# Kernel tuning notes

Hardware: AMD Instinct MI355X
Metric: run time of the kernel (lower is better)

The kernel has to match this reference:

```python
import jax, jax.numpy as jnp
import numpy as np

IGNORE_INDEX = -100
BT, H, V = 2048, 4096, 32000


def setup_inputs() -> dict:
    key = jax.random.key(0)
    k1, k2, k3, k4 = jax.random.split(key, 4)
    _input = jax.random.normal(k1, (BT, H), dtype=jnp.float32) * 0.02
    lin_weight = jax.random.normal(k2, (V, H), dtype=jnp.float32) * 0.02
    bias = jnp.zeros((V,), dtype=jnp.float32)
    target = jax.random.randint(k3, (BT,), 0, V)
    loss_weights = jax.random.uniform(k4, (BT,), dtype=jnp.float32)
    reduce_sum_loss_weights = jnp.sum(loss_weights)  # scalar float32
    return {
        "lin_weight": lin_weight,
        "_input": _input,
        "target": target,
        "bias": bias,
        "loss_weights": loss_weights,
        "reduce_sum_loss_weights": reduce_sum_loss_weights,
        "grad_accumulation_steps": 1,
    }


def reference(lin_weight, _input, target, bias, loss_weights,
              reduce_sum_loss_weights, grad_accumulation_steps):
    # logits: (BT, V) -- the torch module chunks over BT to avoid materializing
    # this; as a correctness reference we compute it directly.
    logits = _input @ lin_weight.T + bias
    mask = target != IGNORE_INDEX                      # (BT,)
    n_non_ignore = jnp.maximum(mask.sum(), 1).astype(logits.dtype)
    safe_t = jnp.where(mask, target, 0)
    lse = jax.nn.logsumexp(logits, axis=-1)            # (BT,)
    gold = jnp.take_along_axis(logits, safe_t[:, None], axis=-1)[:, 0]
    # liger kernel with reduction='mean' divides per-row loss by n_non_ignore
    loss_1d = jnp.where(mask, (lse - gold) / n_non_ignore, 0.0)
    total = jnp.sum(loss_1d * loss_weights)
    rs = jnp.asarray(reduce_sum_loss_weights).reshape(())
    denom = jnp.where(rs == 0, 1.0, rs)
    loss = jnp.where(rs == 0, 0.0, total / denom)
    return loss / grad_accumulation_steps
```

## Files before the change

### kernel.cpp

```cpp
#include <hip/hip_runtime.h>
#include <hip/hip_bf16.h>
#include <math.h>

#define IGNORE_INDEX (-100)

constexpr int BT = 2048, H = 4096, V = 32000;
constexpr int BM = 256, BN = 256, BK = 64;
constexpr int KT = H / BK;
constexpr int MT2 = BT / BM;
constexpr int NT2 = V / BN;
constexpr int NCHUNK = NT2 * 4;

typedef int   i32x4  __attribute__((ext_vector_type(4)));
typedef int   i32x8  __attribute__((ext_vector_type(8)));
typedef float f32x16 __attribute__((ext_vector_type(16)));

#define SC8 120

__device__ __forceinline__ void gload_lds16(const char* g, char* l) {
  __builtin_amdgcn_global_load_lds(
      (const __attribute__((address_space(1))) unsigned int*)(g),
      (__attribute__((address_space(3))) unsigned int*)(l), 16, 0, 0);
}

#define BAR()        asm volatile("s_barrier" ::: "memory")
#define WAIT_VM(N)   asm volatile("s_waitcnt vmcnt(" #N ")" ::: "memory")

__global__ __launch_bounds__(256)
void convert_fp8(const float* __restrict__ src, char* __restrict__ dst,
                 int n8) {
  int i = blockIdx.x * blockDim.x + threadIdx.x;
  const int stride = gridDim.x * blockDim.x;
  for (; i < n8; i += stride) {
    const float4 f0 = ((const float4*)src)[2 * i];
    const float4 f1 = ((const float4*)src)[2 * i + 1];
    const float S = 128.f;
    int lo = 0, hi = 0;
    lo = __builtin_amdgcn_cvt_pk_fp8_f32(f0.x * S, f0.y * S, lo, false);
    lo = __builtin_amdgcn_cvt_pk_fp8_f32(f0.z * S, f0.w * S, lo, true);
    hi = __builtin_amdgcn_cvt_pk_fp8_f32(f1.x * S, f1.y * S, hi, false);
    hi = __builtin_amdgcn_cvt_pk_fp8_f32(f1.z * S, f1.w * S, hi, true);
    int2 v; v.x = lo; v.y = hi;
    ((int2*)dst)[i] = v;
  }
}

__global__ __launch_bounds__(512, 2)
void gemm_lse_fp8(const char* __restrict__ Wq,
                  const char* __restrict__ Xq,
                  const int* __restrict__ target,
                  const float* __restrict__ bias,
                  float* __restrict__ pM, float* __restrict__ pS,
                  float* __restrict__ gold)
{
  __shared__ char As[32768];
  __shared__ char Bs[32768];

  const int tid  = threadIdx.x;
  const int lane = tid & 63;
  const int wid  = tid >> 6;
  const int wr   = wid >> 2;
  const int wcol = wid & 3;

  const int bid = (int)blockIdx.x;
  const int swz = (bid & 7) * 125 + (bid >> 3);
  const int mt = swz & (MT2 - 1);
  const int nt = swz >> 3;
  const int m0 = mt * BM, n0 = nt * BN;

  const int l31 = lane & 31;
  const int h   = lane >> 5;
  const int r2  = (l31 >> 1) & 3;
  const int s0  = ((2 * h) ^ r2) << 4;
  const int s1  = ((2 * h + 1) ^ r2) << 4;
  const int abase = (wr * 128 + l31) * 64;
  const int bbase = (wcol * 64 + l31) * 64;

  const int srow  = lane >> 2;
  const int sslot = ((lane & 3) ^ ((lane >> 3) & 3)) << 4;

  const char* asrc = Xq + (size_t)(m0 + wid * 32 + srow) * H + sslot;
  const char* bsrc = Wq + (size_t)(n0 + wid * 32 + srow) * H + sslot;

  f32x16 acc[4][2] = {};
  i32x8 aF0, aF1, bF0, bF1;

#define STAGE_A(BUF, DT)                                                      \
  { gload_lds16(asrc + (DT) * BK,                                             \
                &As[(BUF) * 16384 + wid * 2048 + lane * 16]);                 \
    gload_lds16(asrc + (size_t)16 * H + (DT) * BK,                            \
                &As[(BUF) * 16384 + wid * 2048 + 1024 + lane * 16]); }

#define STAGE_B(BUF, DT)                                                      \
  { gload_lds16(bsrc + (DT) * BK,                                             \
                &Bs[(BUF) * 16384 + wid * 2048 + lane * 16]);                 \
    gload_lds16(bsrc + (size_t)16 * H + (DT) * BK,                            \
                &Bs[(BUF) * 16384 + wid * 2048 + 1024 + lane * 16]); }

#define RDA(DST, BUF, MI)                                                     \
  { i32x4 lo = *(const i32x4*)&As[(BUF) * 16384 + abase + (MI) * 2048 + s0];  \
    i32x4 hi = *(const i32x4*)&As[(BUF) * 16384 + abase + (MI) * 2048 + s1];  \
    DST[0] = lo[0]; DST[1] = lo[1]; DST[2] = lo[2]; DST[3] = lo[3];           \
    DST[4] = hi[0]; DST[5] = hi[1]; DST[6] = hi[2]; DST[7] = hi[3]; }

#define RDB(DST, BUF, NJ)                                                     \
  { i32x4 lo = *(const i32x4*)&Bs[(BUF) * 16384 + bbase + (NJ) * 2048 + s0];  \
    i32x4 hi = *(const i32x4*)&Bs[(BUF) * 16384 + bbase + (NJ) * 2048 + s1];  \
    DST[0] = lo[0]; DST[1] = lo[1]; DST[2] = lo[2]; DST[3] = lo[3];           \
    DST[4] = hi[0]; DST[5] = hi[1]; DST[6] = hi[2]; DST[7] = hi[3]; }

#define MFMA4(MH)                                                             \
  { __builtin_amdgcn_s_setprio(1);                                            \
    acc[(MH)*2+0][0] = __builtin_amdgcn_mfma_scale_f32_32x32x64_f8f6f4(       \
        aF0, bF0, acc[(MH)*2+0][0], 0, 0, 0, SC8, 0, SC8);                    \
    acc[(MH)*2+0][1] = __builtin_amdgcn_mfma_scale_f32_32x32x64_f8f6f4(       \
        aF0, bF1, acc[(MH)*2+0][1], 0, 0, 0, SC8, 0, SC8);                    \
    acc[(MH)*2+1][0] = __builtin_amdgcn_mfma_scale_f32_32x32x64_f8f6f4(       \
        aF1, bF0, acc[(MH)*2+1][0], 0, 0, 0, SC8, 0, SC8);                    \
    acc[(MH)*2+1][1] = __builtin_amdgcn_mfma_scale_f32_32x32x64_f8f6f4(       \
        aF1, bF1, acc[(MH)*2+1][1], 0, 0, 0, SC8, 0, SC8);                    \
    __builtin_amdgcn_s_setprio(0); }

  STAGE_B(0, 0); STAGE_A(0, 0);

  for (int t = 0; t <= KT - 4; t += 2) {
    STAGE_B(1, 1);
    WAIT_VM(2); BAR();
    RDA(aF0, 0, 0); RDA(aF1, 0, 1); RDB(bF0, 0, 0); RDB(bF1, 0, 1);
    MFMA4(0);
    STAGE_A(1, 1);
    WAIT_VM(2); BAR();
    RDA(aF0, 0, 2); RDA(aF1, 0, 3);
    MFMA4(1);
    STAGE_B(0, 2);
    WAIT_VM(2); BAR();
    RDA(aF0, 1, 0); RDA(aF1, 1, 1); RDB(bF0, 1, 0); RDB(bF1, 1, 1);
    MFMA4(0);
    STAGE_A(0, 2);
    WAIT_VM(2); BAR();
    RDA(aF0, 1, 2); RDA(aF1, 1, 3);
    MFMA4(1);

    asrc += 2 * BK; bsrc += 2 * BK;
  }

  STAGE_B(1, 1);
  WAIT_VM(2); BAR();
  RDA(aF0, 0, 0); RDA(aF1, 0, 1); RDB(bF0, 0, 0); RDB(bF1, 0, 1);
  MFMA4(0);
  STAGE_A(1, 1);
  WAIT_VM(2); BAR();
  RDA(aF0, 0, 2); RDA(aF1, 0, 3);
  MFMA4(1);
  WAIT_VM(0); BAR();
  RDA(aF0, 1, 0); RDA(aF1, 1, 1); RDB(bF0, 1, 0); RDB(bF1, 1, 1);
  MFMA4(0);
  RDA(aF0, 1, 2); RDA(aF1, 1, 3);
  MFMA4(1);

#undef STAGE_A
#undef STAGE_B
#undef RDA
#undef RDB
#undef MFMA4

  const int colbase = n0 + wcol * 64;
  float bv[2];
#pragma unroll
  for (int nj = 0; nj < 2; ++nj) bv[nj] = bias[colbase + nj * 32 + l31];

  const int chunk = nt * 4 + wcol;
#pragma unroll
  for (int mi = 0; mi < 4; ++mi) {
#pragma unroll
    for (int r = 0; r < 16; ++r) {
      const int row = m0 + wr * 128 + mi * 32 + (r & 3) + 8 * (r >> 2) + 4 * h;
      const float v0 = acc[mi][0][r] + bv[0];
      const float v1 = acc[mi][1][r] + bv[1];
      float mx = fmaxf(v0, v1);
#pragma unroll
      for (int d = 1; d < 32; d <<= 1) mx = fmaxf(mx, __shfl_xor(mx, d));
      float s = expf(v0 - mx) + expf(v1 - mx);
#pragma unroll
      for (int d = 1; d < 32; d <<= 1) s += __shfl_xor(s, d);
      if (l31 == 0) {
        pM[(size_t)row * NCHUNK + chunk] = mx;
        pS[(size_t)row * NCHUNK + chunk] = s;
      }
      const int t = target[row];
      const int d0 = t - colbase;
      if (d0 >= 0 && d0 < 64 && l31 == (d0 & 31)) {
        gold[row] = (d0 >> 5) ? v1 : v0;
      }
    }
  }
}

__global__ __launch_bounds__(256)
void reduce_lse(const float* __restrict__ pM, const float* __restrict__ pS,
                const float* __restrict__ gold, const int* __restrict__ target,
                const float* __restrict__ lw, float* __restrict__ rowterm)
{
  const int wid = threadIdx.x >> 6, lane = threadIdx.x & 63;
  const int row = blockIdx.x * 4 + wid;
  if (row >= BT) return;
  const float* pm = pM + (size_t)row * NCHUNK;
  const float* ps = pS + (size_t)row * NCHUNK;
  float m = -INFINITY;
  for (int c2 = lane; c2 < NCHUNK; c2 += 64) m = fmaxf(m, pm[c2]);
#pragma unroll
  for (int d = 1; d < 64; d <<= 1) m = fmaxf(m, __shfl_xor(m, d));
  float s = 0.f;
  for (int c2 = lane; c2 < NCHUNK; c2 += 64) s += ps[c2] * expf(pm[c2] - m);
#pragma unroll
  for (int d = 1; d < 64; d <<= 1) s += __shfl_xor(s, d);
  if (lane == 0) {
    const int t = target[row];
    float term = 0.f;
    if (t != IGNORE_INDEX) term = (m + logf(s) - gold[row]) * lw[row];
    rowterm[row] = term;
  }
}

__global__ __launch_bounds__(256)
void finalize(const float* __restrict__ rowterm, const int* __restrict__ target,
              const float* __restrict__ rsw, const int* __restrict__ gas,
              float* __restrict__ out)
{
  __shared__ float sred[4];
  __shared__ int cred[4];
  const int tid = threadIdx.x;
  float s = 0.f;
  int cnt = 0;
  for (int i = tid; i < BT; i += 256) {
    s += rowterm[i];
    cnt += (target[i] != IGNORE_INDEX) ? 1 : 0;
  }
#pragma unroll
  for (int d = 1; d < 64; d <<= 1) {
    s += __shfl_xor(s, d);
    cnt += __shfl_xor(cnt, d);
  }
  const int wid = tid >> 6, lane = tid & 63;
  if (lane == 0) { sred[wid] = s; cred[wid] = cnt; }
  __syncthreads();
  if (tid == 0) {
    const float st = sred[0] + sred[1] + sred[2] + sred[3];
    const int ct = cred[0] + cred[1] + cred[2] + cred[3];
    const float n = (float)((ct > 0) ? ct : 1);
    const float rs = rsw[0];
    float loss = (rs == 0.f) ? 0.f : (st / n) / rs;
    loss /= (float)gas[0];
    out[0] = loss;
  }
}

extern "C" void kernel_launch(void* const* d_in, const int* in_sizes, int n_in,
                              void* d_out, int out_size, void* d_ws, size_t ws_size,
                              hipStream_t stream)
{
  const float* Wt     = (const float*)d_in[0];
  const float* X      = (const float*)d_in[1];
  const int*   target = (const int*)d_in[2];
  const float* bias   = (const float*)d_in[3];
  const float* lw     = (const float*)d_in[4];
  const float* rsw    = (const float*)d_in[5];
  const int*   gas    = (const int*)d_in[6];
  float* out = (float*)d_out;

  const size_t nW = (size_t)V * H, nX = (size_t)BT * H;

  char* Wq = (char*)d_ws;
  char* Xq = Wq + nW;
  float* pM = (float*)(Xq + nX);
  float* pS = pM + (size_t)BT * NCHUNK;
  float* gold = pS + (size_t)BT * NCHUNK;
  float* rowterm = gold + BT;

  convert_fp8<<<dim3(2048), dim3(256), 0, stream>>>(Wt, Wq, (int)(nW / 8));
  convert_fp8<<<dim3(256), dim3(256), 0, stream>>>(X, Xq, (int)(nX / 8));
  gemm_lse_fp8<<<dim3(MT2 * NT2), dim3(512), 0, stream>>>(Wq, Xq, target,
                                                          bias, pM, pS, gold);
  reduce_lse<<<dim3(BT / 4), dim3(256), 0, stream>>>(pM, pS, gold, target, lw,
                                                     rowterm);
  finalize<<<dim3(1), dim3(256), 0, stream>>>(rowterm, target, rsw, gas, out);
}
```

Before: 549.0 us.

## Load A operand directly from pre-tiled fp8 global layout, bypassing LDS

The X conversion kernel now writes fp8 data in an MFMA-fragment-tiled layout, so each lane can read its A fragment straight from global memory as contiguous 32-byte loads. The GEMM drops the A shared-memory buffer and its staging, keeps only B in LDS, and double-buffers A fragments in registers, prefetching them one K step ahead. This aims to cut LDS traffic and barriers, at the cost of more registers (two sets of four i32x8 A fragments) and global-load latency exposure on A. Since the A tile is reused by many blocks, it relies on L2 hits.

```diff
diff --git a/kernel.cpp b/kernel.cpp
--- a/kernel.cpp
+++ b/kernel.cpp
@@ -25,6 +25,7 @@
 
 #define BAR()        asm volatile("s_barrier" ::: "memory")
 #define WAIT_VM(N)   asm volatile("s_waitcnt vmcnt(" #N ")" ::: "memory")
+#define SB0()        __builtin_amdgcn_sched_barrier(0)
 
 __global__ __launch_bounds__(256)
 void convert_fp8(const float* __restrict__ src, char* __restrict__ dst,
@@ -45,15 +46,38 @@
   }
 }
 
+__global__ __launch_bounds__(256)
+void convert_x_fp8_tiled(const float* __restrict__ src,
+                         char* __restrict__ dst, int n8) {
+  int i = blockIdx.x * blockDim.x + threadIdx.x;
+  const int stride = gridDim.x * blockDim.x;
+  for (; i < n8; i += stride) {
+    const float4 f0 = ((const float4*)src)[2 * i];
+    const float4 f1 = ((const float4*)src)[2 * i + 1];
+    const float S = 128.f;
+    int lo = 0, hi = 0;
+    lo = __builtin_amdgcn_cvt_pk_fp8_f32(f0.x * S, f0.y * S, lo, false);
+    lo = __builtin_amdgcn_cvt_pk_fp8_f32(f0.z * S, f0.w * S, lo, true);
+    hi = __builtin_amdgcn_cvt_pk_fp8_f32(f1.x * S, f1.y * S, hi, false);
+    hi = __builtin_amdgcn_cvt_pk_fp8_f32(f1.z * S, f1.w * S, hi, true);
+    int2 v; v.x = lo; v.y = hi;
+    const int r  = i >> 9;
+    const int k0 = (i & 511) * 8;
+    const int lane = (r & 31) + ((k0 >> 5) & 1) * 32;
+    const size_t addr =
+        ((size_t)((r >> 5) * 64 + (k0 >> 6)) * 64 + lane) * 32 + (k0 & 31);
+    *(int2*)(dst + addr) = v;
+  }
+}
+
 __global__ __launch_bounds__(512, 2)
-void gemm_lse_fp8(const char* __restrict__ Wq,
-                  const char* __restrict__ Xq,
-                  const int* __restrict__ target,
-                  const float* __restrict__ bias,
-                  float* __restrict__ pM, float* __restrict__ pS,
-                  float* __restrict__ gold)
-{
-  __shared__ char As[32768];
+void gemm_lse_adirect(const char* __restrict__ Wq,
+                      const char* __restrict__ Xt,
+                      const int* __restrict__ target,
+                      const float* __restrict__ bias,
+                      float* __restrict__ pM, float* __restrict__ pS,
+                      float* __restrict__ gold)
+{
   __shared__ char Bs[32768];
 
   const int tid  = threadIdx.x;
@@ -73,35 +97,23 @@
   const int r2  = (l31 >> 1) & 3;
   const int s0  = ((2 * h) ^ r2) << 4;
   const int s1  = ((2 * h + 1) ^ r2) << 4;
-  const int abase = (wr * 128 + l31) * 64;
   const int bbase = (wcol * 64 + l31) * 64;
 
   const int srow  = lane >> 2;
   const int sslot = ((lane & 3) ^ ((lane >> 3) & 3)) << 4;
-
-  const char* asrc = Xq + (size_t)(m0 + wid * 32 + srow) * H + sslot;
   const char* bsrc = Wq + (size_t)(n0 + wid * 32 + srow) * H + sslot;
 
-  f32x16 acc[4][2] = {};
-  i32x8 aF0, aF1, bF0, bF1;
-
-#define STAGE_A(BUF, DT)                                                      \
-  { gload_lds16(asrc + (DT) * BK,                                             \
-                &As[(BUF) * 16384 + wid * 2048 + lane * 16]);                 \
-    gload_lds16(asrc + (size_t)16 * H + (DT) * BK,                            \
-                &As[(BUF) * 16384 + wid * 2048 + 1024 + lane * 16]); }
-
-#define STAGE_B(BUF, DT)                                                      \
-  { gload_lds16(bsrc + (DT) * BK,                                             \
+  const int rg0 = mt * 8 + wr * 4;
+  const int aoff = lane * 32;
+
+  f32x16 acc[8] = {};
+  i32x8 aC[4], aN[4], bF0, bF1;
+
+#define STAGE_B(BUF, T)                                                       \
+  { gload_lds16(bsrc + (T) * BK,                                              \
                 &Bs[(BUF) * 16384 + wid * 2048 + lane * 16]);                 \
-    gload_lds16(bsrc + (size_t)16 * H + (DT) * BK,                            \
+    gload_lds16(bsrc + (size_t)16 * H + (T) * BK,                             \
                 &Bs[(BUF) * 16384 + wid * 2048 + 1024 + lane * 16]); }
-
-#define RDA(DST, BUF, MI)                                                     \
-  { i32x4 lo = *(const i32x4*)&As[(BUF) * 16384 + abase + (MI) * 2048 + s0];  \
-    i32x4 hi = *(const i32x4*)&As[(BUF) * 16384 + abase + (MI) * 2048 + s1];  \
-    DST[0] = lo[0]; DST[1] = lo[1]; DST[2] = lo[2]; DST[3] = lo[3];           \
-    DST[4] = hi[0]; DST[5] = hi[1]; DST[6] = hi[2]; DST[7] = hi[3]; }
 
 #define RDB(DST, BUF, NJ)                                                     \
   { i32x4 lo = *(const i32x4*)&Bs[(BUF) * 16384 + bbase + (NJ) * 2048 + s0];  \
@@ -109,60 +121,56 @@
     DST[0] = lo[0]; DST[1] = lo[1]; DST[2] = lo[2]; DST[3] = lo[3];           \
     DST[4] = hi[0]; DST[5] = hi[1]; DST[6] = hi[2]; DST[7] = hi[3]; }
 
-#define MFMA4(MH)                                                             \
+#define LOADA(DST, T)                                                         \
+  { _Pragma("unroll")                                                         \
+    for (int mi = 0; mi < 4; ++mi) {                                          \
+      const char* ap = Xt + ((size_t)((rg0 + mi) * 64 + (T)) << 11) + aoff;   \
+      i32x4 lo = *(const i32x4*)(ap);                                         \
+      i32x4 hi = *(const i32x4*)(ap + 16);                                    \
+      DST[mi][0]=lo[0]; DST[mi][1]=lo[1]; DST[mi][2]=lo[2]; DST[mi][3]=lo[3]; \
+      DST[mi][4]=hi[0]; DST[mi][5]=hi[1]; DST[mi][6]=hi[2]; DST[mi][7]=hi[3]; \
+    } }
+
+#define MFMA8(ASET)                                                           \
   { __builtin_amdgcn_s_setprio(1);                                            \
-    acc[(MH)*2+0][0] = __builtin_amdgcn_mfma_scale_f32_32x32x64_f8f6f4(       \
-        aF0, bF0, acc[(MH)*2+0][0], 0, 0, 0, SC8, 0, SC8);                    \
-    acc[(MH)*2+0][1] = __builtin_amdgcn_mfma_scale_f32_32x32x64_f8f6f4(       \
-        aF0, bF1, acc[(MH)*2+0][1], 0, 0, 0, SC8, 0, SC8);                    \
-    acc[(MH)*2+1][0] = __builtin_amdgcn_mfma_scale_f32_32x32x64_f8f6f4(       \
-        aF1, bF0, acc[(MH)*2+1][0], 0, 0, 0, SC8, 0, SC8);                    \
-    acc[(MH)*2+1][1] = __builtin_amdgcn_mfma_scale_f32_32x32x64_f8f6f4(       \
-        aF1, bF1, acc[(MH)*2+1][1], 0, 0, 0, SC8, 0, SC8);                    \
+    _Pragma("unroll")                                                         \
+    for (int mi = 0; mi < 4; ++mi) {                                          \
+      acc[mi*2+0] = __builtin_amdgcn_mfma_scale_f32_32x32x64_f8f6f4(          \
+          ASET[mi], bF0, acc[mi*2+0], 0, 0, 0, SC8, 0, SC8);                  \
+      acc[mi*2+1] = __builtin_amdgcn_mfma_scale_f32_32x32x64_f8f6f4(          \
+          ASET[mi], bF1, acc[mi*2+1], 0, 0, 0, SC8, 0, SC8);                  \
+    }                                                                         \
     __builtin_amdgcn_s_setprio(0); }
 
-  STAGE_B(0, 0); STAGE_A(0, 0);
-
-  for (int t = 0; t <= KT - 4; t += 2) {
-    STAGE_B(1, 1);
-    WAIT_VM(2); BAR();
-    RDA(aF0, 0, 0); RDA(aF1, 0, 1); RDB(bF0, 0, 0); RDB(bF1, 0, 1);
-    MFMA4(0);
-    STAGE_A(1, 1);
-    WAIT_VM(2); BAR();
-    RDA(aF0, 0, 2); RDA(aF1, 0, 3);
-    MFMA4(1);
-    STAGE_B(0, 2);
-    WAIT_VM(2); BAR();
-    RDA(aF0, 1, 0); RDA(aF1, 1, 1); RDB(bF0, 1, 0); RDB(bF1, 1, 1);
-    MFMA4(0);
-    STAGE_A(0, 2);
-    WAIT_VM(2); BAR();
-    RDA(aF0, 1, 2); RDA(aF1, 1, 3);
-    MFMA4(1);
-
-    asrc += 2 * BK; bsrc += 2 * BK;
-  }
-
-  STAGE_B(1, 1);
-  WAIT_VM(2); BAR();
-  RDA(aF0, 0, 0); RDA(aF1, 0, 1); RDB(bF0, 0, 0); RDB(bF1, 0, 1);
-  MFMA4(0);
-  STAGE_A(1, 1);
-  WAIT_VM(2); BAR();
-  RDA(aF0, 0, 2); RDA(aF1, 0, 3);
-  MFMA4(1);
-  WAIT_VM(0); BAR();
-  RDA(aF0, 1, 0); RDA(aF1, 1, 1); RDB(bF0, 1, 0); RDB(bF1, 1, 1);
-  MFMA4(0);
-  RDA(aF0, 1, 2); RDA(aF1, 1, 3);
-  MFMA4(1);
-
-#undef STAGE_A
+  LOADA(aC, 0);
+  STAGE_B(0, 0);
+  WAIT_VM(0);
+  BAR();
+
+  for (int t = 0; t < KT - 2; t += 2) {
+    STAGE_B(1, t + 1);
+    RDB(bF0, 0, 0); RDB(bF1, 0, 1);
+    LOADA(aN, t + 1);
+    MFMA8(aC);
+    SB0(); WAIT_VM(8); BAR();
+    STAGE_B(0, t + 2);
+    RDB(bF0, 1, 0); RDB(bF1, 1, 1);
+    LOADA(aC, t + 2);
+    MFMA8(aN);
+    SB0(); WAIT_VM(8); BAR();
+  }
+  STAGE_B(1, KT - 1);
+  RDB(bF0, 0, 0); RDB(bF1, 0, 1);
+  LOADA(aN, KT - 1);
+  MFMA8(aC);
+  SB0(); WAIT_VM(8); BAR();
+  RDB(bF0, 1, 0); RDB(bF1, 1, 1);
+  MFMA8(aN);
+
 #undef STAGE_B
-#undef RDA
 #undef RDB
-#undef MFMA4
+#undef LOADA
+#undef MFMA8
 
   const int colbase = n0 + wcol * 64;
   float bv[2];
@@ -175,8 +183,8 @@
 #pragma unroll
     for (int r = 0; r < 16; ++r) {
       const int row = m0 + wr * 128 + mi * 32 + (r & 3) + 8 * (r >> 2) + 4 * h;
-      const float v0 = acc[mi][0][r] + bv[0];
-      const float v1 = acc[mi][1][r] + bv[1];
+      const float v0 = acc[mi * 2 + 0][r] + bv[0];
+      const float v1 = acc[mi * 2 + 1][r] + bv[1];
       float mx = fmaxf(v0, v1);
 #pragma unroll
       for (int d = 1; d < 32; d <<= 1) mx = fmaxf(mx, __shfl_xor(mx, d));
@@ -271,16 +279,18 @@
   const size_t nW = (size_t)V * H, nX = (size_t)BT * H;
 
   char* Wq = (char*)d_ws;
-  char* Xq = Wq + nW;
-  float* pM = (float*)(Xq + nX);
+  char* Xt = Wq + nW;
+  float* pM = (float*)(Xt + nX);
   float* pS = pM + (size_t)BT * NCHUNK;
   float* gold = pS + (size_t)BT * NCHUNK;
   float* rowterm = gold + BT;
 
   convert_fp8<<<dim3(2048), dim3(256), 0, stream>>>(Wt, Wq, (int)(nW / 8));
-  convert_fp8<<<dim3(256), dim3(256), 0, stream>>>(X, Xq, (int)(nX / 8));
-  gemm_lse_fp8<<<dim3(MT2 * NT2), dim3(512), 0, stream>>>(Wq, Xq, target,
-                                                          bias, pM, pS, gold);
+  convert_x_fp8_tiled<<<dim3(1024), dim3(256), 0, stream>>>(X, Xt,
+                                                            (int)(nX / 8));
+  gemm_lse_adirect<<<dim3(MT2 * NT2), dim3(512), 0, stream>>>(Wq, Xt, target,
+                                                              bias, pM, pS,
+                                                              gold);
   reduce_lse<<<dim3(BT / 4), dim3(256), 0, stream>>>(pM, pS, gold, target, lw,
                                                      rowterm);
   finalize<<<dim3(1), dim3(256), 0, stream>>>(rowterm, target, rsw, gas, out);
```

Result: slower. 565.6 us (+3.0%).

## Switch fp8 GEMM main loop to triple-buffered LDS pipeline with one barrier per stage

Applied to the files above, without the earlier changes.

The fused GEMM+logsumexp kernel moves from a two-slot LDS ring with a barrier per half-tile to a three-slot ring. Each K-step issues loads two tiles ahead, waits on vmcnt, runs all MFMAs for the current tile, then takes a single barrier. The goal is deeper prefetch and fewer barriers, so global-to-LDS latency is better hidden behind MFMA work. The cost is 96 KB of LDS per block instead of 64 KB, which may stop two 512-thread blocks from fitting per CU and so reduce occupancy.

```diff
diff --git a/kernel.cpp b/kernel.cpp
--- a/kernel.cpp
+++ b/kernel.cpp
@@ -25,6 +25,7 @@
 
 #define BAR()        asm volatile("s_barrier" ::: "memory")
 #define WAIT_VM(N)   asm volatile("s_waitcnt vmcnt(" #N ")" ::: "memory")
+#define SB0()        __builtin_amdgcn_sched_barrier(0)
 
 __global__ __launch_bounds__(256)
 void convert_fp8(const float* __restrict__ src, char* __restrict__ dst,
@@ -46,15 +47,15 @@
 }
 
 __global__ __launch_bounds__(512, 2)
-void gemm_lse_fp8(const char* __restrict__ Wq,
-                  const char* __restrict__ Xq,
-                  const int* __restrict__ target,
-                  const float* __restrict__ bias,
-                  float* __restrict__ pM, float* __restrict__ pS,
-                  float* __restrict__ gold)
-{
-  __shared__ char As[32768];
-  __shared__ char Bs[32768];
+void gemm_lse_3buf(const char* __restrict__ Wq,
+                   const char* __restrict__ Xq,
+                   const int* __restrict__ target,
+                   const float* __restrict__ bias,
+                   float* __restrict__ pM, float* __restrict__ pS,
+                   float* __restrict__ gold)
+{
+  __shared__ char As[49152];
+  __shared__ char Bs[49152];
 
   const int tid  = threadIdx.x;
   const int lane = tid & 63;
@@ -121,43 +122,37 @@
         aF1, bF1, acc[(MH)*2+1][1], 0, 0, 0, SC8, 0, SC8);                    \
     __builtin_amdgcn_s_setprio(0); }
 
+#define PHASE(D, DOSTAGE, VMN)                                                \
+  { if (DOSTAGE) { STAGE_B(((D) + 2) % 3, (D) + 2);                           \
+                   STAGE_A(((D) + 2) % 3, (D) + 2); }                         \
+    WAIT_VM(VMN);                                                             \
+    RDA(aF0, (D) % 3, 0); RDA(aF1, (D) % 3, 1);                               \
+    RDB(bF0, (D) % 3, 0); RDB(bF1, (D) % 3, 1);                               \
+    MFMA4(0);                                                                 \
+    RDA(aF0, (D) % 3, 2); RDA(aF1, (D) % 3, 3);                               \
+    MFMA4(1);                                                                 \
+    SB0(); BAR(); }
+
   STAGE_B(0, 0); STAGE_A(0, 0);
-
-  for (int t = 0; t <= KT - 4; t += 2) {
-    STAGE_B(1, 1);
-    WAIT_VM(2); BAR();
-    RDA(aF0, 0, 0); RDA(aF1, 0, 1); RDB(bF0, 0, 0); RDB(bF1, 0, 1);
-    MFMA4(0);
-    STAGE_A(1, 1);
-    WAIT_VM(2); BAR();
-    RDA(aF0, 0, 2); RDA(aF1, 0, 3);
-    MFMA4(1);
-    STAGE_B(0, 2);
-    WAIT_VM(2); BAR();
-    RDA(aF0, 1, 0); RDA(aF1, 1, 1); RDB(bF0, 1, 0); RDB(bF1, 1, 1);
-    MFMA4(0);
-    STAGE_A(0, 2);
-    WAIT_VM(2); BAR();
-    RDA(aF0, 1, 2); RDA(aF1, 1, 3);
-    MFMA4(1);
-
-    asrc += 2 * BK; bsrc += 2 * BK;
-  }
-
-  STAGE_B(1, 1);
-  WAIT_VM(2); BAR();
+  STAGE_B(1, 1); STAGE_A(1, 1);
+  WAIT_VM(4);
+  BAR();
+
+  for (int it = 0; it < 20; ++it) {
+    PHASE(0, 1, 4);
+    PHASE(1, 1, 4);
+    PHASE(2, 1, 4);
+    asrc += 3 * BK; bsrc += 3 * BK;
+  }
+  PHASE(0, 1, 4);
+  PHASE(1, 1, 0);
+  PHASE(2, 0, 0);
   RDA(aF0, 0, 0); RDA(aF1, 0, 1); RDB(bF0, 0, 0); RDB(bF1, 0, 1);
   MFMA4(0);
-  STAGE_A(1, 1);
-  WAIT_VM(2); BAR();
   RDA(aF0, 0, 2); RDA(aF1, 0, 3);
   MFMA4(1);
-  WAIT_VM(0); BAR();
-  RDA(aF0, 1, 0); RDA(aF1, 1, 1); RDB(bF0, 1, 0); RDB(bF1, 1, 1);
-  MFMA4(0);
-  RDA(aF0, 1, 2); RDA(aF1, 1, 3);
-  MFMA4(1);
-
+
+#undef PHASE
 #undef STAGE_A
 #undef STAGE_B
 #undef RDA
@@ -279,8 +274,8 @@
 
   convert_fp8<<<dim3(2048), dim3(256), 0, stream>>>(Wt, Wq, (int)(nW / 8));
   convert_fp8<<<dim3(256), dim3(256), 0, stream>>>(X, Xq, (int)(nX / 8));
-  gemm_lse_fp8<<<dim3(MT2 * NT2), dim3(512), 0, stream>>>(Wq, Xq, target,
-                                                          bias, pM, pS, gold);
+  gemm_lse_3buf<<<dim3(MT2 * NT2), dim3(512), 0, stream>>>(Wq, Xq, target,
+                                                           bias, pM, pS, gold);
   reduce_lse<<<dim3(BT / 4), dim3(256), 0, stream>>>(pM, pS, gold, target, lw,
                                                      rowterm);
   finalize<<<dim3(1), dim3(256), 0, stream>>>(rowterm, target, rsw, gas, out);
```

After: 600.5 us. +9.4%, slower.
